# Kernel tuning notes

Hardware: AMD Instinct MI355X
Metric: run time of the kernel (lower is better)

## Reference

```python
import math
import jax, jax.numpy as jnp
import numpy as np

HIDDEN = 1024
NUM_HEADS = 16
HEAD_DIM = HIDDEN // NUM_HEADS
B, S = 4, 2048


def setup_inputs() -> dict:
    key = jax.random.key(0)
    ks = jax.random.split(key, 10)
    sc_in = 1.0 / math.sqrt(HIDDEN)
    inp = {
        "query": jax.random.normal(ks[0], (B, S, HIDDEN), jnp.float32),
        "key": jax.random.normal(ks[1], (B, S, HIDDEN), jnp.float32),
        "value": jax.random.normal(ks[2], (B, S, HIDDEN), jnp.float32),
        "mask": jax.random.randint(ks[3], (B, S), 0, 2).astype(bool),
        # NOTE: ModuleList([Linear]*num_heads) shares ONE Linear across all heads.
        "Wq": jax.random.normal(ks[4], (HIDDEN, HEAD_DIM), jnp.float32) * sc_in,
        "bq": jnp.zeros((HEAD_DIM,), jnp.float32),
        "Wk": jax.random.normal(ks[5], (HIDDEN, HEAD_DIM), jnp.float32) * sc_in,
        "bk": jnp.zeros((HEAD_DIM,), jnp.float32),
        "Wv": jax.random.normal(ks[6], (HIDDEN, HEAD_DIM), jnp.float32) * sc_in,
        "bv": jnp.zeros((HEAD_DIM,), jnp.float32),
        "Wout": jax.random.normal(ks[7], (HIDDEN, HIDDEN), jnp.float32) * sc_in,
        "bout": jnp.zeros((HIDDEN,), jnp.float32),
        "seq_mask": 0,
    }
    return inp


def _layer_norm_scores(x, eps=1e-8):
    # torch.std is unbiased (ddof=1); is_train=False => no affine
    mean = jnp.mean(x, axis=-1, keepdims=True)
    sigma = jnp.std(x, axis=-1, keepdims=True, ddof=1)
    return (x - mean) / (sigma + eps)


def reference(query, key, value, mask, Wq, bq, Wk, bk, Wv, bv, Wout, bout, seq_mask):
    # All heads share identical weights -> compute one head, tile the concat.
    q = query @ Wq + bq          # [B,S,hd]
    k = key @ Wk + bk            # [B,S,hd]
    v = value @ Wv + bv          # [B,S,hd]
    scores = jnp.einsum("bqd,bkd->bqk", q, k) / math.sqrt(HIDDEN)  # [B,S,S]
    scores = _layer_norm_scores(scores)
    m = jnp.broadcast_to(mask[:, None, :], scores.shape)  # [B,S,S]
    if seq_mask:
        tri = jnp.triu(jnp.ones(scores.shape[-2:], bool), k=1)
        m = m | tri[None]
    # original fills with -1e-32 (effectively a no-op bug) -- reproduce exactly
    scores = scores + jnp.where(m, jnp.float32(-1e-32), jnp.float32(0.0))
    attn = jax.nn.softmax(scores, axis=-1)
    head = jnp.einsum("bqk,bkd->bqd", attn, v)   # [B,S,hd]
    attention = jnp.tile(head, (1, 1, NUM_HEADS))  # concat of identical heads
    return attention @ Wout + bout
```

## Files before the change

kernel.cpp:

```cpp
#include <hip/hip_runtime.h>
#include <math.h>

#define B_  4
#define S_  2048
#define H_  1024
#define D_  64
#define ROWS (B_*S_)
#define KSPLIT 8
#define LOG2E 1.4426950408889634f

typedef __attribute__((ext_vector_type(4))) float  floatx4;
typedef __attribute__((ext_vector_type(8))) short  short8;
typedef __attribute__((ext_vector_type(8))) __bf16 bf16x8;

#define WS_KSUM 0
#define WS_M    (WS_KSUM + B_*D_)
#define WS_A2   (WS_M + B_*D_*D_)
#define WS_C2   (WS_A2 + ROWS)
#define WS_SWP  (WS_C2 + ROWS)
#define WS_FEND (WS_SWP + KSPLIT*ROWS)
#define WB_QB  0
#define WB_KF  (WB_QB + ROWS*D_)
#define WB_VF  (WB_KF + ROWS*D_)
#define WB_WT  (WB_VF + ROWS*D_)
#define WB_WFF (WB_WT + 3*D_*H_)
#define WB_HNF (WB_WFF + H_*D_)
#define WB_OP  (WB_HNF + ROWS*D_)
#define NZ2    (B_*D_ + B_*D_*D_)

__device__ __forceinline__ unsigned short f2bf(float f) {
    union { float f; unsigned u; } v; v.f = f;
    unsigned r = v.u + 0x7FFFu + ((v.u >> 16) & 1u);
    return (unsigned short)(r >> 16);
}
__device__ __forceinline__ short bfc(float f) {
    __bf16 h = (__bf16)f;
    short s; __builtin_memcpy(&s, &h, 2); return s;
}
__device__ __forceinline__ float bf2f(short s) {
    union { unsigned u; float f; } v;
    v.u = ((unsigned)(unsigned short)s) << 16; return v.f;
}
__device__ __forceinline__ bf16x8 ldb(const short* p) {
    union { short8 s; bf16x8 b; } u; u.s = *(const short8*)p; return u.b;
}
#define MFMA(a,b,c) __builtin_amdgcn_mfma_f32_16x16x32_bf16(a, b, c, 0, 0, 0)
__device__ __forceinline__ void lds_fence() {
    __builtin_amdgcn_wave_barrier();
    __builtin_amdgcn_s_waitcnt(0xc07f);
    __builtin_amdgcn_wave_barrier();
}

__global__ __launch_bounds__(256) void prep(
    const float* __restrict__ Wq, const float* __restrict__ Wk,
    const float* __restrict__ Wv, const float* __restrict__ Wout,
    float* __restrict__ wsf)
{
    __shared__ float tile[64][65];
    short* wsb = (short*)(wsf + WS_FEND);
    const int bx = blockIdx.x, t = threadIdx.x;
    if (bx < 96) {
        int idx = bx * 256 + t;
        int mat = idx >> 13, rem = idx & 8191;
        int kc = rem >> 8, nt = (rem >> 6) & 3, lane = rem & 63;
        int g = lane >> 4, l15 = lane & 15;
        const float* W = (mat == 0) ? Wq : (mat == 1) ? Wk : Wv;
        short8 fr;
        #pragma unroll
        for (int j = 0; j < 8; ++j)
            fr[j] = (short)f2bf(W[(size_t)(kc*32 + g*8 + j) * D_ + nt*16 + l15]);
        *(short8*)&wsb[WB_WT + (size_t)idx * 8] = fr;
    } else if (bx < 112) {
        int n0 = (bx - 96) * 64;
        int nn = t & 63, dg = t >> 6;
        for (int dd = 0; dd < 16; ++dd) {
            int d = dg * 16 + dd;
            float s = 0.0f;
            #pragma unroll
            for (int h = 0; h < 16; ++h)
                s += Wout[(size_t)(h * 64 + d) * H_ + n0 + nn];
            tile[d][nn] = s;
        }
        __syncthreads();
        #pragma unroll
        for (int u = 0; u < 2; ++u) {
            int s = 2*t + u;
            int ctl = s >> 7, h = (s >> 6) & 1, lane = s & 63;
            int g = lane >> 4, l2 = lane & 15;
            short8 fr;
            #pragma unroll
            for (int j = 0; j < 8; ++j)
                fr[j] = (short)f2bf(tile[h*32 + g*8 + j][ctl*16 + l2]);
            *(short8*)&wsb[WB_WFF + (size_t)((((n0 >> 4) + ctl)*2 + h)*64 + lane) * 8] = fr;
        }
    } else {
        int i = (bx - 112) * 256 + t;
        if (i < NZ2) wsf[WS_KSUM + i] = 0.0f;
    }
}

__global__ __launch_bounds__(256) void qkv_mfma(
    const float* __restrict__ query, const float* __restrict__ key,
    const float* __restrict__ value,
    const float* __restrict__ bq, const float* __restrict__ bk,
    const float* __restrict__ bvp, float* __restrict__ wsf)
{
    short* wsb = (short*)(wsf + WS_FEND);
    const int mat = blockIdx.y;
    const float* X    = (mat == 0) ? query : (mat == 1) ? key : value;
    const float* bias = (mat == 0) ? bq    : (mat == 1) ? bk  : bvp;
    const short* WT3 = wsb + WB_WT + (size_t)mat * (D_ * H_);

    const int t = threadIdx.x, w = t >> 6, lane = t & 63;
    const int l15 = lane & 15, g = lane >> 4;
    const int r0 = blockIdx.x * 32;
    const int mrow0 = (w >> 1) * 16;
    const int nt0 = (w & 1) * 2;

    __shared__ short xs[32][136];
    floatx4 acc[2] = {};

    for (int step = 0; step < 8; ++step) {
        __syncthreads();
        #pragma unroll
        for (int u = 0; u < 4; ++u) {
            int row = u * 8 + (t >> 5), col = (t & 31) * 4;
            float4 xv = *(const float4*)&X[(size_t)(r0 + row) * H_ + step * 128 + col];
            short4 pk;
            pk.x = bfc(xv.x); pk.y = bfc(xv.y); pk.z = bfc(xv.z); pk.w = bfc(xv.w);
            *(short4*)&xs[row][col] = pk;
        }
        __syncthreads();
        #pragma unroll
        for (int kk = 0; kk < 4; ++kk) {
            bf16x8 a = ldb(&xs[mrow0 + l15][kk * 32 + g * 8]);
            int kc = step * 4 + kk;
            #pragma unroll
            for (int n = 0; n < 2; ++n) {
                bf16x8 bf = ldb(&WT3[(size_t)((kc * 4) + nt0 + n) * 512 + lane * 8]);
                acc[n] = MFMA(a, bf, acc[n]);
            }
        }
    }

    if (mat == 0) {
        short* QB = wsb + WB_QB;
        #pragma unroll
        for (int n = 0; n < 2; ++n) {
            int col = (nt0 + n) * 16 + l15;
            float bb = bias[col];
            #pragma unroll
            for (int r = 0; r < 4; ++r)
                QB[(size_t)(r0 + mrow0 + 4*g + r) * D_ + col] = (short)f2bf(acc[n][r] + bb);
        }
    } else if (mat == 1) {
        short* KF = wsb + WB_KF;
        #pragma unroll
        for (int n = 0; n < 2; ++n) {
            int d = (nt0 + n) * 16 + l15;
            int kh = d >> 5, gk = (d >> 3) & 3, j = d & 7;
            float bb = bias[d];
            #pragma unroll
            for (int r = 0; r < 4; ++r) {
                int R = r0 + mrow0 + 4*g + r;
                KF[(size_t)(((R >> 4) * 2 + kh) * 64 + gk * 16 + (R & 15)) * 8 + j] =
                    (short)f2bf(acc[n][r] + bb);
            }
        }
    } else {
        short* VF = wsb + WB_VF;
        int R0 = r0 + mrow0 + 4*g;
        int kh = (R0 >> 5) & 1, gv = (R0 >> 3) & 3, j0 = R0 & 7, blk = R0 >> 6;
        #pragma unroll
        for (int n = 0; n < 2; ++n) {
            int d = (nt0 + n) * 16 + l15;
            int ntv = d >> 4;
            float bb = bias[d];
            short4 pk;
            pk.x = (short)f2bf(acc[n][0] + bb); pk.y = (short)f2bf(acc[n][1] + bb);
            pk.z = (short)f2bf(acc[n][2] + bb); pk.w = (short)f2bf(acc[n][3] + bb);
            *(short4*)&VF[(size_t)(((blk * 4 + ntv) * 2 + kh) * 64 + gv * 16 + (d & 15)) * 8 + j0] = pk;
        }
    }
}

__global__ __launch_bounds__(256) void kstats(float* __restrict__ wsf) {
    const short* KF = (short*)(wsf + WS_FEND) + WB_KF;
    const int b     = blockIdx.x >> 5;
    const int chunk = blockIdx.x & 31;
    const int keyblk0 = b * 128 + chunk * 4;

    __shared__ float kt[64][64];
    const int t = threadIdx.x;
    #pragma unroll
    for (int u = 0; u < 2; ++u) {
        int s = 2*t + u;
        int kb4 = s >> 7, kh = (s >> 6) & 1, lane2 = s & 63;
        int g2 = lane2 >> 4, l2 = lane2 & 15;
        short8 v = *(const short8*)&KF[(size_t)(((keyblk0 + kb4) * 2 + kh) * 64 + lane2) * 8];
        #pragma unroll
        for (int j = 0; j < 8; ++j)
            kt[kb4 * 16 + l2][kh * 32 + g2 * 8 + j] = bf2f(v[j]);
    }
    __syncthreads();

    const int td = t >> 4, te = t & 15;
    float acc[4][4] = {};
    for (int j = 0; j < 64; ++j) {
        float4 a  = *(const float4*)&kt[j][td*4];
        float4 bb = *(const float4*)&kt[j][te*4];
        float av[4] = {a.x, a.y, a.z, a.w};
        float bw[4] = {bb.x, bb.y, bb.z, bb.w};
        #pragma unroll
        for (int i = 0; i < 4; ++i)
            #pragma unroll
            for (int l = 0; l < 4; ++l)
                acc[i][l] += av[i] * bw[l];
    }
    float* M = wsf + WS_M + (size_t)b * D_ * D_;
    #pragma unroll
    for (int i = 0; i < 4; ++i)
        #pragma unroll
        for (int l = 0; l < 4; ++l)
            atomicAdd(&M[(td*4 + i) * D_ + te*4 + l], acc[i][l]);

    if (t < 64) {
        float s = 0.0f;
        for (int j = 0; j < 64; ++j) s += kt[j][t];
        atomicAdd(&wsf[WS_KSUM + b * D_ + t], s);
    }
}

__global__ __launch_bounds__(256) void rowstats(float* __restrict__ wsf) {
    const short* Qb = (short*)(wsf + WS_FEND) + WB_QB;
    const int t = threadIdx.x, w = t >> 6, lane = t & 63;
    const int q0 = blockIdx.x * 32 + w * 8;
    const int b  = q0 >> 11;
    const float* M = wsf + WS_M + (size_t)b * D_ * D_;

    float qv[8], y[8] = {};
    #pragma unroll
    for (int r = 0; r < 8; ++r) qv[r] = bf2f(Qb[(size_t)(q0 + r) * D_ + lane]);
    for (int d2 = 0; d2 < 64; ++d2) {
        float m = M[d2 * D_ + lane];
        #pragma unroll
        for (int r = 0; r < 8; ++r) y[r] += __shfl(qv[r], d2, 64) * m;
    }
    float kl = wsf[WS_KSUM + b * D_ + lane];
    float z[8], sv[8];
    #pragma unroll
    for (int r = 0; r < 8; ++r) { z[r] = y[r] * qv[r]; sv[r] = qv[r] * kl; }
    #pragma unroll
    for (int m = 1; m < 64; m <<= 1) {
        #pragma unroll
        for (int r = 0; r < 8; ++r) {
            z[r]  += __shfl_xor(z[r],  m, 64);
            sv[r] += __shfl_xor(sv[r], m, 64);
        }
    }
    #pragma unroll
    for (int r = 0; r < 8; ++r) {
        if (lane == r) {
            float sum   = sv[r] * (1.0f / 32.0f);
            float sumsq = z[r]  * (1.0f / 1024.0f);
            float mu  = sum * (1.0f / 2048.0f);
            float var = (sumsq - sum * sum * (1.0f / 2048.0f)) * (1.0f / 2047.0f);
            var = fmaxf(var, 0.0f);
            float inv = 1.0f / (sqrtf(var) + 1e-8f);
            wsf[WS_A2 + q0 + r] = inv * (LOG2E / 32.0f);
            wsf[WS_C2 + q0 + r] = -mu * inv * LOG2E;
        }
    }
}

__global__ __launch_bounds__(256) void attention(float* __restrict__ wsf) {
    short* wsb = (short*)(wsf + WS_FEND);
    const short* Qb = wsb + WB_QB;
    const short* KF = wsb + WB_KF;
    const short* VF = wsb + WB_VF;
    __shared__ short P[4][32][72];

    const int t = threadIdx.x, w = t >> 6, lane = t & 63;
    const int l15 = lane & 15, g = lane >> 4;
    const int q0 = blockIdx.x * 128 + w * 32;
    const int b  = blockIdx.x >> 4;
    const int kb = blockIdx.y * (S_ / KSPLIT);

    bf16x8 bqf[2][2];
    float a2v[2], c2v[2];
    #pragma unroll
    for (int nt = 0; nt < 2; ++nt) {
        int q = q0 + nt*16 + l15;
        #pragma unroll
        for (int h = 0; h < 2; ++h)
            bqf[nt][h] = ldb(&Qb[(size_t)q * D_ + h*32 + g*8]);
        a2v[nt] = wsf[WS_A2 + q];
        c2v[nt] = wsf[WS_C2 + q];
    }

    floatx4 O[2][4] = {};
    float sacc[2] = {0.0f, 0.0f};
    short* Pw = &P[w][0][0];

    for (int kc = 0; kc < S_ / KSPLIT; kc += 64) {
        const int key0 = kb + kc;
        const int kblk16 = (b * S_ + key0) >> 4;
        const int kblk64 = (b * S_ + key0) >> 6;
        floatx4 Sc[4][2] = {};
        #pragma unroll
        for (int kt = 0; kt < 4; ++kt) {
            bf16x8 ak0 = ldb(&KF[(size_t)(((kblk16 + kt) * 2 + 0) * 64 + lane) * 8]);
            bf16x8 ak1 = ldb(&KF[(size_t)(((kblk16 + kt) * 2 + 1) * 64 + lane) * 8]);
            #pragma unroll
            for (int nt = 0; nt < 2; ++nt) {
                Sc[kt][nt] = MFMA(ak0, bqf[nt][0], Sc[kt][nt]);
                Sc[kt][nt] = MFMA(ak1, bqf[nt][1], Sc[kt][nt]);
            }
        }
        lds_fence();
        #pragma unroll
        for (int nt = 0; nt < 2; ++nt) {
            const float aa = a2v[nt], cc = c2v[nt];
            #pragma unroll
            for (int kt = 0; kt < 4; ++kt) {
                float w0 = exp2f(fmaf(Sc[kt][nt][0], aa, cc));
                float w1 = exp2f(fmaf(Sc[kt][nt][1], aa, cc));
                float w2 = exp2f(fmaf(Sc[kt][nt][2], aa, cc));
                float w3 = exp2f(fmaf(Sc[kt][nt][3], aa, cc));
                sacc[nt] += (w0 + w1) + (w2 + w3);
                short4 pk;
                pk.x = bfc(w0); pk.y = bfc(w1); pk.z = bfc(w2); pk.w = bfc(w3);
                *(short4*)&Pw[(nt*16 + l15) * 72 + kt*16 + 4*g] = pk;
            }
        }
        lds_fence();
        bf16x8 ap[2][2];
        #pragma unroll
        for (int mt = 0; mt < 2; ++mt)
            #pragma unroll
            for (int kh = 0; kh < 2; ++kh)
                ap[mt][kh] = ldb(&Pw[(mt*16 + l15) * 72 + kh*32 + g*8]);
        #pragma unroll
        for (int nt = 0; nt < 4; ++nt) {
            #pragma unroll
            for (int kh = 0; kh < 2; ++kh) {
                bf16x8 bv = ldb(&VF[(size_t)(((kblk64 * 4 + nt) * 2 + kh) * 64 + lane) * 8]);
                #pragma unroll
                for (int mt = 0; mt < 2; ++mt)
                    O[mt][nt] = MFMA(ap[mt][kh], bv, O[mt][nt]);
            }
        }
    }

    #pragma unroll
    for (int nt = 0; nt < 2; ++nt) {
        sacc[nt] += __shfl_xor(sacc[nt], 16, 64);
        sacc[nt] += __shfl_xor(sacc[nt], 32, 64);
    }
    if (lane < 16) {
        wsf[WS_SWP + blockIdx.y * ROWS + q0 + lane]      = sacc[0];
        wsf[WS_SWP + blockIdx.y * ROWS + q0 + 16 + lane] = sacc[1];
    }
    short* OP = wsb + WB_OP + ((size_t)blockIdx.y * ROWS + q0) * D_;
    #pragma unroll
    for (int mt = 0; mt < 2; ++mt)
        #pragma unroll
        for (int nt = 0; nt < 4; ++nt)
            #pragma unroll
            for (int r = 0; r < 4; ++r)
                OP[(size_t)(mt*16 + 4*g + r) * D_ + nt*16 + l15] =
                    (short)f2bf(O[mt][nt][r]);
}

__global__ __launch_bounds__(256) void reduceo(float* __restrict__ wsf) {
    short* wsb = (short*)(wsf + WS_FEND);
    const short* OP = wsb + WB_OP;
    short* HNF = wsb + WB_HNF;
    const int t = threadIdx.x;
    const int row = blockIdx.x * 32 + (t >> 3);
    const int c8 = (t & 7) * 8;
    float sw = 0.0f;
    #pragma unroll
    for (int p = 0; p < KSPLIT; ++p) sw += wsf[WS_SWP + p * ROWS + row];
    float inv = 1.0f / sw;
    float a[8] = {};
    #pragma unroll
    for (int p = 0; p < KSPLIT; ++p) {
        short8 o = *(const short8*)&OP[((size_t)p * ROWS + row) * D_ + c8];
        #pragma unroll
        for (int j = 0; j < 8; ++j) a[j] += bf2f(o[j]);
    }
    short8 hn;
    #pragma unroll
    for (int j = 0; j < 8; ++j) hn[j] = (short)f2bf(a[j] * inv);
    int kh = c8 >> 5, gH = (c8 >> 3) & 3;
    *(short8*)&HNF[(size_t)(((row >> 4) * 2 + kh) * 64 + gH * 16 + (row & 15)) * 8] = hn;
}

__global__ __launch_bounds__(256) void finalize(
    const float* __restrict__ bout, const float* __restrict__ wsf,
    float* __restrict__ out)
{
    const short* wsb = (const short*)(wsf + WS_FEND);
    const short* HNF = wsb + WB_HNF;
    const short* WFF = wsb + WB_WFF;
    const int t = threadIdx.x, w = t >> 6, lane = t & 63;
    const int l15 = lane & 15, g = lane >> 4;
    const int rowblk = blockIdx.x * 4 + w;
    const int r0 = rowblk * 16;
    const int c0 = blockIdx.y * 64;

    bf16x8 ah[2];
    #pragma unroll
    for (int h = 0; h < 2; ++h)
        ah[h] = ldb(&HNF[(size_t)((rowblk * 2 + h) * 64 + lane) * 8]);

    floatx4 acc[4] = {};
    #pragma unroll
    for (int nt = 0; nt < 4; ++nt) {
        #pragma unroll
        for (int h = 0; h < 2; ++h) {
            bf16x8 bf = ldb(&WFF[(size_t)((((c0 >> 4) + nt) * 2 + h) * 64 + lane) * 8]);
            acc[nt] = MFMA(ah[h], bf, acc[nt]);
        }
    }
    #pragma unroll
    for (int nt = 0; nt < 4; ++nt) {
        int col = c0 + nt*16 + l15;
        float bb = bout[col];
        #pragma unroll
        for (int r = 0; r < 4; ++r)
            out[(size_t)(r0 + 4*g + r) * H_ + col] = acc[nt][r] + bb;
    }
}

extern "C" void kernel_launch(void* const* d_in, const int* in_sizes, int n_in,
                              void* d_out, int out_size, void* d_ws, size_t ws_size,
                              hipStream_t stream) {
    const float* query = (const float*)d_in[0];
    const float* key   = (const float*)d_in[1];
    const float* value = (const float*)d_in[2];
    const float* Wq   = (const float*)d_in[4];
    const float* bq   = (const float*)d_in[5];
    const float* Wk   = (const float*)d_in[6];
    const float* bk   = (const float*)d_in[7];
    const float* Wv   = (const float*)d_in[8];
    const float* bv   = (const float*)d_in[9];
    const float* Wout = (const float*)d_in[10];
    const float* bout = (const float*)d_in[11];

    float* ws  = (float*)d_ws;
    float* out = (float*)d_out;

    prep<<<177, 256, 0, stream>>>(Wq, Wk, Wv, Wout, ws);
    qkv_mfma<<<dim3(ROWS/32, 3), 256, 0, stream>>>(query, key, value, bq, bk, bv, ws);
    kstats<<<B_ * 32, 256, 0, stream>>>(ws);
    rowstats<<<ROWS/32, 256, 0, stream>>>(ws);
    attention<<<dim3(ROWS/128, KSPLIT), 256, 0, stream>>>(ws);
    reduceo<<<ROWS/32, 256, 0, stream>>>(ws);
    finalize<<<dim3(ROWS/64, H_/64), 256, 0, stream>>>(bout, ws, out);
}
```

Before: 211.5 us.

## Stage K/V tiles through double-buffered LDS and fuse split-K reduce into output GEMM

The attention kernel now loads each 64-key K and V chunk cooperatively into a double-buffered shared-memory stage, prefetching the next chunk into registers. All four waves then read it from LDS instead of each wave loading it separately from global memory. The separate reduceo kernel is folded into the output projection: each block reduces the KSPLIT partial outputs for 16 rows into LDS and immediately runs the MFMA against Wout. This removes a launch and the HNF round trip through memory. The trade-offs are more LDS per block, which may limit occupancy, and extra block barriers.

Result: faster. 202.1 us (-4.4%).

```diff
diff --git a/kernel.cpp b/kernel.cpp
--- a/kernel.cpp
+++ b/kernel.cpp
@@ -24,8 +24,7 @@
 #define WB_VF  (WB_KF + ROWS*D_)
 #define WB_WT  (WB_VF + ROWS*D_)
 #define WB_WFF (WB_WT + 3*D_*H_)
-#define WB_HNF (WB_WFF + H_*D_)
-#define WB_OP  (WB_HNF + ROWS*D_)
+#define WB_OP  (WB_WFF + H_*D_)
 #define NZ2    (B_*D_ + B_*D_*D_)
 
 __device__ __forceinline__ unsigned short f2bf(float f) {
@@ -279,6 +278,7 @@
     const short* KF = wsb + WB_KF;
     const short* VF = wsb + WB_VF;
     __shared__ short P[4][32][72];
+    __shared__ short stage[2][8192];
 
     const int t = threadIdx.x, w = t >> 6, lane = t & 63;
     const int l15 = lane & 15, g = lane >> 4;
@@ -302,15 +302,40 @@
     float sacc[2] = {0.0f, 0.0f};
     short* Pw = &P[w][0][0];
 
+    const int tb = t * 8;
+    short8 rr[4];
+    {
+        const short* KFc = KF + (size_t)((b * S_ + kb) >> 4) * 1024;
+        const short* VFc = VF + (size_t)((b * S_ + kb) >> 6) * 4096;
+        rr[0] = *(const short8*)&KFc[tb];
+        rr[1] = *(const short8*)&KFc[tb + 2048];
+        rr[2] = *(const short8*)&VFc[tb];
+        rr[3] = *(const short8*)&VFc[tb + 2048];
+    }
+
     for (int kc = 0; kc < S_ / KSPLIT; kc += 64) {
-        const int key0 = kb + kc;
-        const int kblk16 = (b * S_ + key0) >> 4;
-        const int kblk64 = (b * S_ + key0) >> 6;
+        short* buf = &stage[(kc >> 6) & 1][0];
+        __syncthreads();
+        *(short8*)&buf[tb]        = rr[0];
+        *(short8*)&buf[tb + 2048] = rr[1];
+        *(short8*)&buf[tb + 4096] = rr[2];
+        *(short8*)&buf[tb + 6144] = rr[3];
+        if (kc + 64 < S_ / KSPLIT) {
+            const int key1 = kb + kc + 64;
+            const short* KFc = KF + (size_t)((b * S_ + key1) >> 4) * 1024;
+            const short* VFc = VF + (size_t)((b * S_ + key1) >> 6) * 4096;
+            rr[0] = *(const short8*)&KFc[tb];
+            rr[1] = *(const short8*)&KFc[tb + 2048];
+            rr[2] = *(const short8*)&VFc[tb];
+            rr[3] = *(const short8*)&VFc[tb + 2048];
+        }
+        __syncthreads();
+
         floatx4 Sc[4][2] = {};
         #pragma unroll
         for (int kt = 0; kt < 4; ++kt) {
-            bf16x8 ak0 = ldb(&KF[(size_t)(((kblk16 + kt) * 2 + 0) * 64 + lane) * 8]);
-            bf16x8 ak1 = ldb(&KF[(size_t)(((kblk16 + kt) * 2 + 1) * 64 + lane) * 8]);
+            bf16x8 ak0 = ldb(&buf[(kt*2 + 0)*512 + lane*8]);
+            bf16x8 ak1 = ldb(&buf[(kt*2 + 1)*512 + lane*8]);
             #pragma unroll
             for (int nt = 0; nt < 2; ++nt) {
                 Sc[kt][nt] = MFMA(ak0, bqf[nt][0], Sc[kt][nt]);
@@ -344,7 +369,7 @@
         for (int nt = 0; nt < 4; ++nt) {
             #pragma unroll
             for (int kh = 0; kh < 2; ++kh) {
-                bf16x8 bv = ldb(&VF[(size_t)(((kblk64 * 4 + nt) * 2 + kh) * 64 + lane) * 8]);
+                bf16x8 bv = ldb(&buf[4096 + (nt*2 + kh)*512 + lane*8]);
                 #pragma unroll
                 for (int mt = 0; mt < 2; ++mt)
                     O[mt][nt] = MFMA(ap[mt][kh], bv, O[mt][nt]);
@@ -372,65 +397,54 @@
                     (short)f2bf(O[mt][nt][r]);
 }
 
-__global__ __launch_bounds__(256) void reduceo(float* __restrict__ wsf) {
-    short* wsb = (short*)(wsf + WS_FEND);
-    const short* OP = wsb + WB_OP;
-    short* HNF = wsb + WB_HNF;
-    const int t = threadIdx.x;
-    const int row = blockIdx.x * 32 + (t >> 3);
-    const int c8 = (t & 7) * 8;
-    float sw = 0.0f;
-    #pragma unroll
-    for (int p = 0; p < KSPLIT; ++p) sw += wsf[WS_SWP + p * ROWS + row];
-    float inv = 1.0f / sw;
-    float a[8] = {};
-    #pragma unroll
-    for (int p = 0; p < KSPLIT; ++p) {
-        short8 o = *(const short8*)&OP[((size_t)p * ROWS + row) * D_ + c8];
-        #pragma unroll
-        for (int j = 0; j < 8; ++j) a[j] += bf2f(o[j]);
-    }
-    short8 hn;
-    #pragma unroll
-    for (int j = 0; j < 8; ++j) hn[j] = (short)f2bf(a[j] * inv);
-    int kh = c8 >> 5, gH = (c8 >> 3) & 3;
-    *(short8*)&HNF[(size_t)(((row >> 4) * 2 + kh) * 64 + gH * 16 + (row & 15)) * 8] = hn;
-}
-
-__global__ __launch_bounds__(256) void finalize(
+__global__ __launch_bounds__(256) void outmm(
     const float* __restrict__ bout, const float* __restrict__ wsf,
     float* __restrict__ out)
 {
     const short* wsb = (const short*)(wsf + WS_FEND);
-    const short* HNF = wsb + WB_HNF;
+    const short* OP  = wsb + WB_OP;
     const short* WFF = wsb + WB_WFF;
-    const int t = threadIdx.x, w = t >> 6, lane = t & 63;
-    const int l15 = lane & 15, g = lane >> 4;
-    const int rowblk = blockIdx.x * 4 + w;
-    const int r0 = rowblk * 16;
-    const int c0 = blockIdx.y * 64;
-
-    bf16x8 ah[2];
-    #pragma unroll
-    for (int h = 0; h < 2; ++h)
-        ah[h] = ldb(&HNF[(size_t)((rowblk * 2 + h) * 64 + lane) * 8]);
-
-    floatx4 acc[4] = {};
-    #pragma unroll
-    for (int nt = 0; nt < 4; ++nt) {
-        #pragma unroll
-        for (int h = 0; h < 2; ++h) {
-            bf16x8 bf = ldb(&WFF[(size_t)((((c0 >> 4) + nt) * 2 + h) * 64 + lane) * 8]);
-            acc[nt] = MFMA(ah[h], bf, acc[nt]);
-        }
-    }
-    #pragma unroll
-    for (int nt = 0; nt < 4; ++nt) {
-        int col = c0 + nt*16 + l15;
+    __shared__ short hnF[2 * 64 * 8];
+
+    const int t = threadIdx.x;
+    const int row0 = blockIdx.x * 16;
+
+    {
+        const int r = t >> 4;
+        const int c = (t & 15) * 4;
+        const int row = row0 + r;
+        float sw = 0.0f;
+        #pragma unroll
+        for (int p = 0; p < KSPLIT; ++p) sw += wsf[WS_SWP + p * ROWS + row];
+        float inv = 1.0f / sw;
+        float a0 = 0.f, a1 = 0.f, a2 = 0.f, a3 = 0.f;
+        #pragma unroll
+        for (int p = 0; p < KSPLIT; ++p) {
+            short4 o = *(const short4*)&OP[((size_t)p * ROWS + row) * D_ + c];
+            a0 += bf2f(o.x); a1 += bf2f(o.y); a2 += bf2f(o.z); a3 += bf2f(o.w);
+        }
+        short4 hn;
+        hn.x = (short)f2bf(a0 * inv); hn.y = (short)f2bf(a1 * inv);
+        hn.z = (short)f2bf(a2 * inv); hn.w = (short)f2bf(a3 * inv);
+        int kh = c >> 5, gH = (c >> 3) & 3, j0 = c & 7;
+        *(short4*)&hnF[(size_t)(kh * 64 + gH * 16 + r) * 8 + j0] = hn;
+    }
+    __syncthreads();
+
+    const int w = t >> 6, lane = t & 63, l15 = lane & 15, g = lane >> 4;
+    bf16x8 ah0 = ldb(&hnF[(size_t)(0 * 64 + lane) * 8]);
+    bf16x8 ah1 = ldb(&hnF[(size_t)(1 * 64 + lane) * 8]);
+    #pragma unroll
+    for (int i = 0; i < 16; ++i) {
+        int n16 = w * 16 + i;
+        floatx4 acc = {};
+        acc = MFMA(ah0, ldb(&WFF[(size_t)(n16 * 2 + 0) * 512 + lane * 8]), acc);
+        acc = MFMA(ah1, ldb(&WFF[(size_t)(n16 * 2 + 1) * 512 + lane * 8]), acc);
+        int col = n16 * 16 + l15;
         float bb = bout[col];
         #pragma unroll
         for (int r = 0; r < 4; ++r)
-            out[(size_t)(r0 + 4*g + r) * H_ + col] = acc[nt][r] + bb;
+            out[(size_t)(row0 + 4*g + r) * H_ + col] = acc[r] + bb;
     }
 }
 
@@ -457,6 +471,5 @@
     kstats<<<B_ * 32, 256, 0, stream>>>(ws);
     rowstats<<<ROWS/32, 256, 0, stream>>>(ws);
     attention<<<dim3(ROWS/128, KSPLIT), 256, 0, stream>>>(ws);
-    reduceo<<<ROWS/32, 256, 0, stream>>>(ws);
-    finalize<<<dim3(ROWS/64, H_/64), 256, 0, stream>>>(bout, ws, out);
-}
+    outmm<<<ROWS/16, 256, 0, stream>>>(bout, ws, out);
+}
```
